# Performance work log

Measured on AMD Instinct MI355X. Metric: run time of the kernel, lower is better.

Reference implementation:

```python
import jax, jax.numpy as jnp
import numpy as np

# Reconstructed semantics of the butterfly C++ kernel:
#  - gather rows of `data` via indices_in -> x [N, B]
#  - num_input_layers of Givens-rotation butterfly layers (pairs within 16-wide
#    blocks, XOR stride 1,2,4,8 cycling per layer)
#  - fused bias + smooth-ReLU activation (curvature-smoothed) on the first
#    num_activations rows of each 16-block
#  - num_output_layers more butterfly layers
#  - scatter result back into `data` at idx_out (forward returns data, updated)

COL_BLOCK = 16
NUM_INPUT_LAYERS = 4
NUM_OUTPUT_LAYERS = 4
NUM_ACTIVATIONS = 8
CURVATURE = 0.1


def _rotate_layer(x, ang, stride):
    # x: [N, B]; ang: [N//2]
    N = x.shape[0]
    idx = np.arange(N)
    low = idx[((idx % COL_BLOCK) & stride) == 0]  # static pair indices
    hi = low + stride
    c = jnp.cos(ang)[:, None]
    s = jnp.sin(ang)[:, None]
    xl, xh = x[low], x[hi]
    return x.at[low].set(c * xl + s * xh).at[hi].set(-s * xl + c * xh)


def setup_inputs() -> dict:
    key = jax.random.key(0)
    k1, k2, k3 = jax.random.split(key, 3)
    N, B = 4096, 8192
    num_layers = NUM_INPUT_LAYERS + NUM_OUTPUT_LAYERS
    num_blocks = N // COL_BLOCK
    data = jax.random.normal(k1, (N, B), dtype=jnp.float32)
    angles = jax.random.uniform(k2, (num_layers, N // 2), dtype=jnp.float32,
                                minval=-np.pi, maxval=np.pi)
    biases = jax.random.normal(k3, (NUM_ACTIVATIONS * num_blocks,), dtype=jnp.float32)
    indices_in = jnp.arange(N, dtype=jnp.int32)
    idx_out = jnp.arange(N, dtype=jnp.int32)
    return {"data": data, "angles": angles, "biases": biases,
            "indices_in": indices_in, "idx_out": idx_out}


def reference(data, angles, biases, indices_in, idx_out):
    N = indices_in.shape[0]
    x = data[indices_in]  # [N, B] gather
    layer = 0
    for _ in range(NUM_INPUT_LAYERS):
        x = _rotate_layer(x, angles[layer], 1 << (layer % 4))
        layer += 1
    # fused bias + smooth ReLU on first NUM_ACTIVATIONS rows of each 16-block
    offs = np.arange(N) % COL_BLOCK
    act_rows = np.nonzero(offs < NUM_ACTIVATIONS)[0]  # block-major order matches biases layout
    b_full = jnp.zeros((N,), x.dtype).at[act_rows].set(biases)
    xa = x + b_full[:, None]
    act = 0.5 * (xa + jnp.sqrt(xa * xa + CURVATURE * CURVATURE))
    mask = jnp.asarray(offs < NUM_ACTIVATIONS)[:, None]
    x = jnp.where(mask, act, x)
    for _ in range(NUM_OUTPUT_LAYERS):
        x = _rotate_layer(x, angles[layer], 1 << (layer % 4))
        layer += 1
    return data.at[idx_out].set(x)  # scatter back (mimics in-place update)
```

## Files before the change

### kernel.cpp

```cpp
#include <hip/hip_runtime.h>


constexpr int COL_BLOCK = 16;
constexpr int TPB = 256;
constexpr int CPT = 4;
constexpr int NCHUNK = 2;
constexpr float CURV2 = 0.1f * 0.1f;

typedef float floatx4 __attribute__((ext_vector_type(4)));

template <int L>
__device__ __forceinline__ void rot_layer(floatx4 (&x)[16],
                                          const float (&cs)[8][8],
                                          const float (&sn)[8][8]) {
    constexpr int b = L & 3;
    constexpr int s = 1 << b;
#pragma unroll
    for (int j = 0; j < 8; ++j) {
        const int lo = ((j >> b) << (b + 1)) | (j & (s - 1));
        const int hi = lo + s;
        const float c = cs[L][j];
        const float sv = sn[L][j];
        const floatx4 xl = x[lo];
        const floatx4 xh = x[hi];
        x[lo] = c * xl + sv * xh;
        x[hi] = c * xh - sv * xl;
    }
}

__device__ __forceinline__ void process16(floatx4 (&x)[16],
                                          const float (&cs)[8][8],
                                          const float (&sn)[8][8],
                                          const float (&bs)[8]) {
    rot_layer<0>(x, cs, sn);
    rot_layer<1>(x, cs, sn);
    rot_layer<2>(x, cs, sn);
    rot_layer<3>(x, cs, sn);

#pragma unroll
    for (int j = 0; j < 8; ++j) {
        const float b = bs[j];
        floatx4 v = x[j];
#pragma unroll
        for (int e = 0; e < 4; ++e) {
            const float a = v[e] + b;
            v[e] = 0.5f * (a + sqrtf(fmaf(a, a, CURV2)));
        }
        x[j] = v;
    }

    rot_layer<4>(x, cs, sn);
    rot_layer<5>(x, cs, sn);
    rot_layer<6>(x, cs, sn);
    rot_layer<7>(x, cs, sn);
}

__global__ __launch_bounds__(TPB) void butterfly_kernel2(
    const float* __restrict__ data,
    const float* __restrict__ angles,
    const float* __restrict__ biases,
    const int* __restrict__ indices_in,
    const int* __restrict__ idx_out,
    float* __restrict__ out,
    int N, int B)
{
    const int tile = blockIdx.x;
    const int blk = blockIdx.y;
    const int tid = threadIdx.x;
    const int half = N >> 1;

    __shared__ float cs[8][8];
    __shared__ float sn[8][8];
    __shared__ float bs[8];

    const int l = tid >> 3, jj = tid & 7;
    float ang_v = 0.0f, bias_v = 0.0f;
    if (tid < 64) {
        ang_v = angles[l * half + blk * 8 + jj];
    } else if (tid < 72) {
        bias_v = biases[blk * 8 + (tid - 64)];
    }

    int rin[16], rout[16];
#pragma unroll
    for (int j = 0; j < 16; ++j) rin[j] = indices_in[blk * COL_BLOCK + j];
#pragma unroll
    for (int j = 0; j < 16; ++j) rout[j] = idx_out[blk * COL_BLOCK + j];

    const int c0 = tile * (NCHUNK * TPB * CPT) + tid * CPT;

    floatx4 x[16];
#pragma unroll
    for (int j = 0; j < 16; ++j) {
        const size_t off = (size_t)rin[j] * (size_t)B + (size_t)c0;
        x[j] = *reinterpret_cast<const floatx4*>(data + off);
    }

    if (tid < 64) {
        cs[l][jj] = cosf(ang_v);
        sn[l][jj] = sinf(ang_v);
    } else if (tid < 72) {
        bs[tid - 64] = bias_v;
    }
    __syncthreads();

    process16(x, cs, sn, bs);
#pragma unroll
    for (int j = 0; j < 16; ++j) {
        const size_t off = (size_t)rout[j] * (size_t)B + (size_t)c0;
        *reinterpret_cast<floatx4*>(out + off) = x[j];
    }

    const int c1 = c0 + TPB * CPT;
#pragma unroll
    for (int j = 0; j < 16; ++j) {
        const size_t off = (size_t)rin[j] * (size_t)B + (size_t)c1;
        x[j] = *reinterpret_cast<const floatx4*>(data + off);
    }
    process16(x, cs, sn, bs);
#pragma unroll
    for (int j = 0; j < 16; ++j) {
        const size_t off = (size_t)rout[j] * (size_t)B + (size_t)c1;
        *reinterpret_cast<floatx4*>(out + off) = x[j];
    }
}

__global__ __launch_bounds__(TPB) void butterfly_kernel1(
    const float* __restrict__ data, const float* __restrict__ angles,
    const float* __restrict__ biases, const int* __restrict__ indices_in,
    const int* __restrict__ idx_out, float* __restrict__ out, int N, int B)
{
    const int tile = blockIdx.x;
    const int blk = blockIdx.y;
    const int tid = threadIdx.x;
    const int half = N >> 1;

    __shared__ float cs[8][8];
    __shared__ float sn[8][8];
    __shared__ float bs[8];

    const int l = tid >> 3, jj = tid & 7;
    float ang_v = 0.0f, bias_v = 0.0f;
    if (tid < 64) ang_v = angles[l * half + blk * 8 + jj];
    else if (tid < 72) bias_v = biases[blk * 8 + (tid - 64)];

    int rin[16], rout[16];
#pragma unroll
    for (int j = 0; j < 16; ++j) rin[j] = indices_in[blk * COL_BLOCK + j];
#pragma unroll
    for (int j = 0; j < 16; ++j) rout[j] = idx_out[blk * COL_BLOCK + j];

    const int c0 = tile * (TPB * CPT) + tid * CPT;

    floatx4 x[16];
#pragma unroll
    for (int j = 0; j < 16; ++j) {
        const size_t off = (size_t)rin[j] * (size_t)B + (size_t)c0;
        x[j] = *reinterpret_cast<const floatx4*>(data + off);
    }

    if (tid < 64) { cs[l][jj] = cosf(ang_v); sn[l][jj] = sinf(ang_v); }
    else if (tid < 72) bs[tid - 64] = bias_v;
    __syncthreads();

    process16(x, cs, sn, bs);
#pragma unroll
    for (int j = 0; j < 16; ++j) {
        const size_t off = (size_t)rout[j] * (size_t)B + (size_t)c0;
        *reinterpret_cast<floatx4*>(out + off) = x[j];
    }
}

constexpr int MAX_MASK_N = 1 << 16;
__device__ int g_mask[MAX_MASK_N];

__global__ void zero_mask_kernel(int N) {
    const int i = blockIdx.x * blockDim.x + threadIdx.x;
    if (i < N) g_mask[i] = 0;
}

__global__ void mark_kernel_g(const int* __restrict__ idx_out, int N) {
    const int i = blockIdx.x * blockDim.x + threadIdx.x;
    if (i < N) g_mask[idx_out[i]] = 1;
}

__global__ __launch_bounds__(TPB) void copy_untouched_g(
    const float* __restrict__ data, float* __restrict__ out, int N, int B) {
    for (int row = blockIdx.x; row < N; row += gridDim.x) {
        if (g_mask[row]) continue;
        const floatx4* src = reinterpret_cast<const floatx4*>(data + (size_t)row * B);
        floatx4* dst = reinterpret_cast<floatx4*>(out + (size_t)row * B);
        for (int c = threadIdx.x; c < (B >> 2); c += blockDim.x)
            dst[c] = src[c];
    }
}

__global__ void mark_kernel_ws(const int* __restrict__ idx_out,
                               int* __restrict__ mask, int N) {
    const int i = blockIdx.x * blockDim.x + threadIdx.x;
    if (i < N) mask[idx_out[i]] = 1;
}

__global__ __launch_bounds__(TPB) void copy_untouched_ws(
    const float* __restrict__ data, float* __restrict__ out,
    const int* __restrict__ mask, int N, int B) {
    for (int row = blockIdx.x; row < N; row += gridDim.x) {
        if (mask[row]) continue;
        const floatx4* src = reinterpret_cast<const floatx4*>(data + (size_t)row * B);
        floatx4* dst = reinterpret_cast<floatx4*>(out + (size_t)row * B);
        for (int c = threadIdx.x; c < (B >> 2); c += blockDim.x)
            dst[c] = src[c];
    }
}

extern "C" void kernel_launch(void* const* d_in, const int* in_sizes, int n_in,
                              void* d_out, int out_size, void* d_ws, size_t ws_size,
                              hipStream_t stream) {
    const float* data       = (const float*)d_in[0];
    const float* angles     = (const float*)d_in[1];
    const float* biases     = (const float*)d_in[2];
    const int*   indices_in = (const int*)d_in[3];
    const int*   idx_out    = (const int*)d_in[4];
    float* out = (float*)d_out;

    const int N = in_sizes[3];
    const int B = in_sizes[0] / N;

    const dim3 tpb(TPB);
    const dim3 mgrid((N + TPB - 1) / TPB);

    const bool use_global_mask = (N <= MAX_MASK_N);
    if (use_global_mask) {
        zero_mask_kernel<<<mgrid, tpb, 0, stream>>>(N);
        mark_kernel_g<<<mgrid, tpb, 0, stream>>>(idx_out, N);
    } else {
        int* mask = (int*)d_ws;
        hipMemsetAsync(mask, 0, (size_t)N * sizeof(int), stream);
        mark_kernel_ws<<<mgrid, tpb, 0, stream>>>(idx_out, (int*)d_ws, N);
    }

    if (B % (NCHUNK * TPB * CPT) == 0) {
        dim3 grid(B / (NCHUNK * TPB * CPT), N / COL_BLOCK);
        butterfly_kernel2<<<grid, tpb, 0, stream>>>(
            data, angles, biases, indices_in, idx_out, out, N, B);
    } else {
        dim3 grid(B / (TPB * CPT), N / COL_BLOCK);
        butterfly_kernel1<<<grid, tpb, 0, stream>>>(
            data, angles, biases, indices_in, idx_out, out, N, B);
    }

    if (use_global_mask) {
        copy_untouched_g<<<dim3(256), tpb, 0, stream>>>(data, out, N, B);
    } else {
        copy_untouched_ws<<<dim3(256), tpb, 0, stream>>>(
            data, out, (const int*)d_ws, N, B);
    }
}
```

Baseline: 251.0 us.

## Single-chunk butterfly kernel, fused last layer into stores, shared-memory bitmap copy

Drops the two-chunk-per-block variant in favour of one chunk per block, which doubles the grid. The final rotation layer is now fused directly into the output stores. The mask zero/mark kernels are replaced by a single copy kernel that builds a shared-memory bitmap of idx_out per block, which removes two launches. It also uses the raw amdgcn sqrt builtin and adds a generic scalar fallback; the cost is that every copy block rescans all of idx_out.

New measurement: 244.5 us. 1.03x faster.

```diff
diff --git a/kernel.cpp b/kernel.cpp
--- a/kernel.cpp
+++ b/kernel.cpp
@@ -4,7 +4,6 @@
 constexpr int COL_BLOCK = 16;
 constexpr int TPB = 256;
 constexpr int CPT = 4;
-constexpr int NCHUNK = 2;
 constexpr float CURV2 = 0.1f * 0.1f;
 
 typedef float floatx4 __attribute__((ext_vector_type(4)));
@@ -28,34 +27,7 @@
     }
 }
 
-__device__ __forceinline__ void process16(floatx4 (&x)[16],
-                                          const float (&cs)[8][8],
-                                          const float (&sn)[8][8],
-                                          const float (&bs)[8]) {
-    rot_layer<0>(x, cs, sn);
-    rot_layer<1>(x, cs, sn);
-    rot_layer<2>(x, cs, sn);
-    rot_layer<3>(x, cs, sn);
-
-#pragma unroll
-    for (int j = 0; j < 8; ++j) {
-        const float b = bs[j];
-        floatx4 v = x[j];
-#pragma unroll
-        for (int e = 0; e < 4; ++e) {
-            const float a = v[e] + b;
-            v[e] = 0.5f * (a + sqrtf(fmaf(a, a, CURV2)));
-        }
-        x[j] = v;
-    }
-
-    rot_layer<4>(x, cs, sn);
-    rot_layer<5>(x, cs, sn);
-    rot_layer<6>(x, cs, sn);
-    rot_layer<7>(x, cs, sn);
-}
-
-__global__ __launch_bounds__(TPB) void butterfly_kernel2(
+__global__ __launch_bounds__(TPB) void butterfly_kernel(
     const float* __restrict__ data,
     const float* __restrict__ angles,
     const float* __restrict__ biases,
@@ -87,7 +59,7 @@
 #pragma unroll
     for (int j = 0; j < 16; ++j) rout[j] = idx_out[blk * COL_BLOCK + j];
 
-    const int c0 = tile * (NCHUNK * TPB * CPT) + tid * CPT;
+    const int c0 = tile * (TPB * CPT) + tid * CPT;
 
     floatx4 x[16];
 #pragma unroll
@@ -104,33 +76,45 @@
     }
     __syncthreads();
 
-    process16(x, cs, sn, bs);
-#pragma unroll
-    for (int j = 0; j < 16; ++j) {
-        const size_t off = (size_t)rout[j] * (size_t)B + (size_t)c0;
-        *reinterpret_cast<floatx4*>(out + off) = x[j];
-    }
-
-    const int c1 = c0 + TPB * CPT;
-#pragma unroll
-    for (int j = 0; j < 16; ++j) {
-        const size_t off = (size_t)rin[j] * (size_t)B + (size_t)c1;
-        x[j] = *reinterpret_cast<const floatx4*>(data + off);
-    }
-    process16(x, cs, sn, bs);
-#pragma unroll
-    for (int j = 0; j < 16; ++j) {
-        const size_t off = (size_t)rout[j] * (size_t)B + (size_t)c1;
-        *reinterpret_cast<floatx4*>(out + off) = x[j];
-    }
-}
-
-__global__ __launch_bounds__(TPB) void butterfly_kernel1(
+    rot_layer<0>(x, cs, sn);
+    rot_layer<1>(x, cs, sn);
+    rot_layer<2>(x, cs, sn);
+    rot_layer<3>(x, cs, sn);
+
+#pragma unroll
+    for (int j = 0; j < 8; ++j) {
+        const float b = bs[j];
+        floatx4 v = x[j];
+#pragma unroll
+        for (int e = 0; e < 4; ++e) {
+            const float a = v[e] + b;
+            v[e] = 0.5f * (a + __builtin_amdgcn_sqrtf(fmaf(a, a, CURV2)));
+        }
+        x[j] = v;
+    }
+
+    rot_layer<4>(x, cs, sn);
+    rot_layer<5>(x, cs, sn);
+    rot_layer<6>(x, cs, sn);
+
+#pragma unroll
+    for (int j = 0; j < 8; ++j) {
+        const float c = cs[7][j];
+        const float sv = sn[7][j];
+        const floatx4 xl = x[j];
+        const floatx4 xh = x[j + 8];
+        const floatx4 rlo = c * xl + sv * xh;
+        const floatx4 rhi = c * xh - sv * xl;
+        *reinterpret_cast<floatx4*>(out + (size_t)rout[j] * (size_t)B + (size_t)c0) = rlo;
+        *reinterpret_cast<floatx4*>(out + (size_t)rout[j + 8] * (size_t)B + (size_t)c0) = rhi;
+    }
+}
+
+__global__ __launch_bounds__(TPB) void butterfly_generic(
     const float* __restrict__ data, const float* __restrict__ angles,
     const float* __restrict__ biases, const int* __restrict__ indices_in,
     const int* __restrict__ idx_out, float* __restrict__ out, int N, int B)
 {
-    const int tile = blockIdx.x;
     const int blk = blockIdx.y;
     const int tid = threadIdx.x;
     const int half = N >> 1;
@@ -139,10 +123,15 @@
     __shared__ float sn[8][8];
     __shared__ float bs[8];
 
-    const int l = tid >> 3, jj = tid & 7;
-    float ang_v = 0.0f, bias_v = 0.0f;
-    if (tid < 64) ang_v = angles[l * half + blk * 8 + jj];
-    else if (tid < 72) bias_v = biases[blk * 8 + (tid - 64)];
+    if (tid < 64) {
+        const int l = tid >> 3, j = tid & 7;
+        const float a = angles[l * half + blk * 8 + j];
+        cs[l][j] = cosf(a);
+        sn[l][j] = sinf(a);
+    } else if (tid < 72) {
+        bs[tid - 64] = biases[blk * 8 + (tid - 64)];
+    }
+    __syncthreads();
 
     int rin[16], rout[16];
 #pragma unroll
@@ -150,66 +139,86 @@
 #pragma unroll
     for (int j = 0; j < 16; ++j) rout[j] = idx_out[blk * COL_BLOCK + j];
 
-    const int c0 = tile * (TPB * CPT) + tid * CPT;
-
-    floatx4 x[16];
-#pragma unroll
-    for (int j = 0; j < 16; ++j) {
-        const size_t off = (size_t)rin[j] * (size_t)B + (size_t)c0;
-        x[j] = *reinterpret_cast<const floatx4*>(data + off);
-    }
-
-    if (tid < 64) { cs[l][jj] = cosf(ang_v); sn[l][jj] = sinf(ang_v); }
-    else if (tid < 72) bs[tid - 64] = bias_v;
-    __syncthreads();
-
-    process16(x, cs, sn, bs);
-#pragma unroll
-    for (int j = 0; j < 16; ++j) {
-        const size_t off = (size_t)rout[j] * (size_t)B + (size_t)c0;
-        *reinterpret_cast<floatx4*>(out + off) = x[j];
-    }
-}
-
-constexpr int MAX_MASK_N = 1 << 16;
-__device__ int g_mask[MAX_MASK_N];
+    for (int c = blockIdx.x * TPB + tid; c < B; c += gridDim.x * TPB) {
+        float x[16];
+#pragma unroll
+        for (int j = 0; j < 16; ++j)
+            x[j] = data[(size_t)rin[j] * (size_t)B + c];
+#pragma unroll
+        for (int L = 0; L < 8; ++L) {
+            const int b = L & 3, s = 1 << b;
+#pragma unroll
+            for (int j = 0; j < 8; ++j) {
+                const int lo = ((j >> b) << (b + 1)) | (j & (s - 1));
+                const int hi = lo + s;
+                const float cc = cs[L][j], ss = sn[L][j];
+                const float xl = x[lo], xh = x[hi];
+                x[lo] = cc * xl + ss * xh;
+                x[hi] = cc * xh - ss * xl;
+            }
+            if (L == 3) {
+#pragma unroll
+                for (int j = 0; j < 8; ++j) {
+                    const float a = x[j] + bs[j];
+                    x[j] = 0.5f * (a + sqrtf(fmaf(a, a, CURV2)));
+                }
+            }
+        }
+#pragma unroll
+        for (int j = 0; j < 16; ++j)
+            out[(size_t)rout[j] * (size_t)B + c] = x[j];
+    }
+}
+
+constexpr int MAX_BITMAP_N = 1 << 16;
+
+__global__ __launch_bounds__(TPB) void copy_untouched_fused(
+    const float* __restrict__ data, float* __restrict__ out,
+    const int* __restrict__ idx_out, int N, int B)
+{
+    __shared__ unsigned bm[MAX_BITMAP_N / 32];
+    const int words = (N + 31) >> 5;
+    for (int w = threadIdx.x; w < words; w += TPB) bm[w] = 0u;
+    __syncthreads();
+    for (int i = threadIdx.x; i < N; i += TPB) {
+        const int r = idx_out[i];
+        atomicOr(&bm[r >> 5], 1u << (r & 31));
+    }
+    __syncthreads();
+
+    const int r0 = blockIdx.x * COL_BLOCK;
+#pragma unroll 1
+    for (int j = 0; j < COL_BLOCK; ++j) {
+        const int row = r0 + j;
+        if (row >= N) break;
+        if (bm[row >> 5] & (1u << (row & 31))) continue;
+        if ((B & 3) == 0) {
+            const floatx4* src = reinterpret_cast<const floatx4*>(data + (size_t)row * B);
+            floatx4* dst = reinterpret_cast<floatx4*>(out + (size_t)row * B);
+            for (int c = threadIdx.x; c < (B >> 2); c += TPB) dst[c] = src[c];
+        } else {
+            for (int c = threadIdx.x; c < B; c += TPB)
+                out[(size_t)row * B + c] = data[(size_t)row * B + c];
+        }
+    }
+}
+
+__device__ int g_mask[1 << 22];
 
 __global__ void zero_mask_kernel(int N) {
     const int i = blockIdx.x * blockDim.x + threadIdx.x;
     if (i < N) g_mask[i] = 0;
 }
-
 __global__ void mark_kernel_g(const int* __restrict__ idx_out, int N) {
     const int i = blockIdx.x * blockDim.x + threadIdx.x;
     if (i < N) g_mask[idx_out[i]] = 1;
 }
-
 __global__ __launch_bounds__(TPB) void copy_untouched_g(
     const float* __restrict__ data, float* __restrict__ out, int N, int B) {
     for (int row = blockIdx.x; row < N; row += gridDim.x) {
         if (g_mask[row]) continue;
-        const floatx4* src = reinterpret_cast<const floatx4*>(data + (size_t)row * B);
-        floatx4* dst = reinterpret_cast<floatx4*>(out + (size_t)row * B);
-        for (int c = threadIdx.x; c < (B >> 2); c += blockDim.x)
-            dst[c] = src[c];
-    }
-}
-
-__global__ void mark_kernel_ws(const int* __restrict__ idx_out,
-                               int* __restrict__ mask, int N) {
-    const int i = blockIdx.x * blockDim.x + threadIdx.x;
-    if (i < N) mask[idx_out[i]] = 1;
-}
-
-__global__ __launch_bounds__(TPB) void copy_untouched_ws(
-    const float* __restrict__ data, float* __restrict__ out,
-    const int* __restrict__ mask, int N, int B) {
-    for (int row = blockIdx.x; row < N; row += gridDim.x) {
-        if (mask[row]) continue;
-        const floatx4* src = reinterpret_cast<const floatx4*>(data + (size_t)row * B);
-        floatx4* dst = reinterpret_cast<floatx4*>(out + (size_t)row * B);
-        for (int c = threadIdx.x; c < (B >> 2); c += blockDim.x)
-            dst[c] = src[c];
+        for (int c = threadIdx.x; c < B; c += blockDim.x)
+            out[(size_t)row * B + c] = data[(size_t)row * B + c];
     }
 }
 
@@ -227,32 +236,24 @@
     const int B = in_sizes[0] / N;
 
     const dim3 tpb(TPB);
-    const dim3 mgrid((N + TPB - 1) / TPB);
-
-    const bool use_global_mask = (N <= MAX_MASK_N);
-    if (use_global_mask) {
+
+    if (B % (TPB * CPT) == 0) {
+        dim3 grid(B / (TPB * CPT), N / COL_BLOCK);
+        butterfly_kernel<<<grid, tpb, 0, stream>>>(
+            data, angles, biases, indices_in, idx_out, out, N, B);
+    } else {
+        dim3 grid(64, N / COL_BLOCK);
+        butterfly_generic<<<grid, tpb, 0, stream>>>(
+            data, angles, biases, indices_in, idx_out, out, N, B);
+    }
+
+    if (N <= MAX_BITMAP_N) {
+        dim3 grid((N + COL_BLOCK - 1) / COL_BLOCK);
+        copy_untouched_fused<<<grid, tpb, 0, stream>>>(data, out, idx_out, N, B);
+    } else {
+        const dim3 mgrid((N + TPB - 1) / TPB);
         zero_mask_kernel<<<mgrid, tpb, 0, stream>>>(N);
         mark_kernel_g<<<mgrid, tpb, 0, stream>>>(idx_out, N);
-    } else {
-        int* mask = (int*)d_ws;
-        hipMemsetAsync(mask, 0, (size_t)N * sizeof(int), stream);
-        mark_kernel_ws<<<mgrid, tpb, 0, stream>>>(idx_out, (int*)d_ws, N);
-    }
-
-    if (B % (NCHUNK * TPB * CPT) == 0) {
-        dim3 grid(B / (NCHUNK * TPB * CPT), N / COL_BLOCK);
-        butterfly_kernel2<<<grid, tpb, 0, stream>>>(
-            data, angles, biases, indices_in, idx_out, out, N, B);
-    } else {
-        dim3 grid(B / (TPB * CPT), N / COL_BLOCK);
-        butterfly_kernel1<<<grid, tpb, 0, stream>>>(
-            data, angles, biases, indices_in, idx_out, out, N, B);
-    }
-
-    if (use_global_mask) {
         copy_untouched_g<<<dim3(256), tpb, 0, stream>>>(data, out, N, B);
-    } else {
-        copy_untouched_ws<<<dim3(256), tpb, 0, stream>>>(
-            data, out, (const int*)d_ws, N, B);
-    }
-}
+    }
+}
```
